# Performance work log

Measured on AMD Instinct MI355X. Metric: run time of the kernel, lower is better.

## Reference

```python
import jax, jax.numpy as jnp
import numpy as np

N_NODES = 50000
N_EDGES = 800000
IN_CH = 128
OUT_CH = 32
HEADS = 8
NEG_SLOPE = 0.2


def setup_inputs() -> dict:
    key = jax.random.key(0)
    k1, k2, k3, k4, k5, k6 = jax.random.split(key, 6)
    x = jax.random.normal(k1, (N_NODES, IN_CH), dtype=jnp.float32)
    edge_index = jax.random.randint(k2, (2, N_EDGES), 0, N_NODES, dtype=jnp.int64)
    # Glorot-ish scaled params
    W = jax.random.normal(k3, (IN_CH, HEADS * OUT_CH), dtype=jnp.float32) * (1.0 / np.sqrt(IN_CH))
    att_src = jax.random.normal(k4, (HEADS, OUT_CH), dtype=jnp.float32) * (1.0 / np.sqrt(OUT_CH))
    att_dst = jax.random.normal(k5, (HEADS, OUT_CH), dtype=jnp.float32) * (1.0 / np.sqrt(OUT_CH))
    bias = jax.random.normal(k6, (HEADS * OUT_CH,), dtype=jnp.float32) * 0.01
    return {"x": x, "edge_index": edge_index, "W": W, "att_src": att_src, "att_dst": att_dst, "bias": bias}


def reference(x, edge_index, W, att_src, att_dst, bias):
    N = x.shape[0]
    # PyG GATConv default: add self loops
    loops = jnp.arange(N, dtype=edge_index.dtype)
    src = jnp.concatenate([edge_index[0], loops])  # message source j
    dst = jnp.concatenate([edge_index[1], loops])  # message destination i

    # Linear projection: [N, H, C]
    h = (x @ W).reshape(N, HEADS, OUT_CH)

    # Per-node attention logits per head: [N, H]
    a_src = jnp.einsum('nhc,hc->nh', h, att_src)
    a_dst = jnp.einsum('nhc,hc->nh', h, att_dst)

    # Per-edge scores: [E, H]
    e = jax.nn.leaky_relu(a_src[src] + a_dst[dst], NEG_SLOPE)

    # Segment softmax over edges sharing a destination (self loops guarantee non-empty segments)
    e_max = jax.ops.segment_max(e, dst, num_segments=N)
    e_exp = jnp.exp(e - e_max[dst])
    e_sum = jax.ops.segment_sum(e_exp, dst, num_segments=N)
    alpha = e_exp / (e_sum[dst] + 1e-16)  # [E, H]

    # Weighted message aggregation: [N, H, C] -> concat heads [N, H*C]
    msg = h[src] * alpha[:, :, None]
    out = jax.ops.segment_sum(msg, dst, num_segments=N).reshape(N, HEADS * OUT_CH)
    out = out + bias
    # unlinear = ReLU (act='relu', norm=None)
    return jax.nn.relu(out)
```

## Files before the change

### kernel.cpp

```cpp
#include <hip/hip_runtime.h>

#define IN_CH 128
#define OUT_CH 32
#define HEADS 8
#define HC 256
#define NEG_SLOPE 0.2f

typedef __attribute__((ext_vector_type(8))) short short8;
typedef __attribute__((ext_vector_type(4))) float f32x4;

__device__ __forceinline__ float bflo(unsigned u) { return __uint_as_float(u << 16); }
__device__ __forceinline__ float bfhi(unsigned u) { return __uint_as_float(u & 0xffff0000u); }
__device__ __forceinline__ float bf2f(unsigned short u) { return __uint_as_float(((unsigned)u) << 16); }
__device__ __forceinline__ unsigned short f2bf(float f) {
    unsigned u = __float_as_uint(f);
    u = (u + 0x7fffu + ((u >> 16) & 1u)) >> 16;
    return (unsigned short)u;
}

__global__ __launch_bounds__(256)
void gat_prep(const float* __restrict__ W, unsigned short* __restrict__ Wt,
              int* __restrict__ counts, int n)
{
    const int idx = blockIdx.x * 256 + threadIdx.x;
    const int k = idx >> 8;
    const int col = idx & 255;
    Wt[col * IN_CH + k] = f2bf(W[idx]);
    for (int i = idx; i < n; i += 32768) counts[i] = 0;
}

__global__ __launch_bounds__(256)
void gat_proj_mfma(const float* __restrict__ x, const unsigned short* __restrict__ Wt,
                   const float* __restrict__ attS, const float* __restrict__ attD,
                   unsigned short* __restrict__ h, float* __restrict__ aS,
                   float* __restrict__ aD, int N)
{
    __shared__ unsigned short lbuf[32 * 264];

    const int tid = threadIdx.x;
    const int lane = tid & 63;
    const int w = tid >> 6;
    const int row0 = blockIdx.x * 32;

#pragma unroll
    for (int u = 0; u < 2; ++u) {
        const int unit = tid + u * 256;
        const int srow = unit >> 4;
        const int sseg = unit & 15;
        const int grow = row0 + srow;
        float4 v0 = make_float4(0.f, 0.f, 0.f, 0.f), v1 = v0;
        if (grow < N) {
            const float* xp = x + (size_t)grow * IN_CH + sseg * 8;
            v0 = *(const float4*)xp;
            v1 = *(const float4*)(xp + 4);
        }
        short8 pk;
        pk[0] = (short)f2bf(v0.x); pk[1] = (short)f2bf(v0.y);
        pk[2] = (short)f2bf(v0.z); pk[3] = (short)f2bf(v0.w);
        pk[4] = (short)f2bf(v1.x); pk[5] = (short)f2bf(v1.y);
        pk[6] = (short)f2bf(v1.z); pk[7] = (short)f2bf(v1.w);
        *(short8*)&lbuf[srow * 136 + sseg * 8] = pk;
    }
    __syncthreads();

    const unsigned short* wp = Wt + (size_t)(w * 64 + (lane & 15)) * IN_CH
                                  + ((lane >> 4) << 3);

    f32x4 acc[2][4];
#pragma unroll
    for (int m = 0; m < 2; ++m)
#pragma unroll
        for (int i = 0; i < 4; ++i) acc[m][i] = (f32x4){0.f, 0.f, 0.f, 0.f};

#pragma unroll
    for (int ks = 0; ks < 4; ++ks) {
        short8 bfr[4];
#pragma unroll
        for (int i = 0; i < 4; ++i)
            bfr[i] = *(const short8*)(wp + i * 16 * IN_CH + ks * 32);
#pragma unroll
        for (int m = 0; m < 2; ++m) {
            const short8 a = *(const short8*)&lbuf[((lane & 15) + m * 16) * 136
                                                   + ks * 32 + ((lane >> 4) << 3)];
#pragma unroll
            for (int i = 0; i < 4; ++i)
                acc[m][i] = __builtin_amdgcn_mfma_f32_16x16x32_bf16(a, bfr[i], acc[m][i], 0, 0, 0);
        }
    }

    const int rbase = (lane >> 4) << 2;
    float ps[2][2][4], pd[2][2][4];
#pragma unroll
    for (int m = 0; m < 2; ++m)
#pragma unroll
        for (int hp = 0; hp < 2; ++hp)
#pragma unroll
            for (int r = 0; r < 4; ++r) { ps[m][hp][r] = 0.f; pd[m][hp][r] = 0.f; }

#pragma unroll
    for (int i = 0; i < 4; ++i) {
        const int hp = i >> 1;
        const float asv = attS[(w * 2 + hp) * 32 + (i & 1) * 16 + (lane & 15)];
        const float adv = attD[(w * 2 + hp) * 32 + (i & 1) * 16 + (lane & 15)];
#pragma unroll
        for (int m = 0; m < 2; ++m)
#pragma unroll
            for (int r = 0; r < 4; ++r) {
                ps[m][hp][r] = fmaf(acc[m][i][r], asv, ps[m][hp][r]);
                pd[m][hp][r] = fmaf(acc[m][i][r], adv, pd[m][hp][r]);
            }
    }
#pragma unroll
    for (int off = 1; off < 16; off <<= 1) {
#pragma unroll
        for (int m = 0; m < 2; ++m)
#pragma unroll
            for (int hp = 0; hp < 2; ++hp)
#pragma unroll
                for (int r = 0; r < 4; ++r) {
                    ps[m][hp][r] += __shfl_xor(ps[m][hp][r], off, 64);
                    pd[m][hp][r] += __shfl_xor(pd[m][hp][r], off, 64);
                }
    }
    if ((lane & 15) == 0) {
#pragma unroll
        for (int m = 0; m < 2; ++m)
#pragma unroll
            for (int hp = 0; hp < 2; ++hp)
#pragma unroll
                for (int r = 0; r < 4; ++r) {
                    const int grow = row0 + m * 16 + rbase + r;
                    if (grow < N) {
                        aS[grow * HEADS + w * 2 + hp] = ps[m][hp][r];
                        aD[grow * HEADS + w * 2 + hp] = pd[m][hp][r];
                    }
                }
    }

    __syncthreads();
#pragma unroll
    for (int i = 0; i < 4; ++i) {
        const int col = w * 64 + i * 16 + (lane & 15);
#pragma unroll
        for (int m = 0; m < 2; ++m)
#pragma unroll
            for (int r = 0; r < 4; ++r)
                lbuf[(m * 16 + rbase + r) * 264 + col] = f2bf(acc[m][i][r]);
    }
    __syncthreads();

#pragma unroll
    for (int u = 0; u < 4; ++u) {
        const int unit = u * 256 + tid;
        const int srow = unit >> 5;
        const int sseg = unit & 31;
        const int grow = row0 + srow;
        if (grow < N)
            *(short8*)(h + (size_t)grow * HC + sseg * 8) =
                *(const short8*)&lbuf[srow * 264 + sseg * 8];
    }
}

__global__ __launch_bounds__(256)
void gat_hist(const int* __restrict__ dst, int* __restrict__ counts,
              int* __restrict__ rank, int E)
{
    int i = (blockIdx.x * 256 + threadIdx.x) * 8;
    if (i + 7 < E) {
        const int4 d0 = *(const int4*)&dst[i];
        const int4 d1 = *(const int4*)&dst[i + 4];
        int4 r0, r1;
        r0.x = atomicAdd(&counts[d0.x], 1);
        r0.y = atomicAdd(&counts[d0.y], 1);
        r0.z = atomicAdd(&counts[d0.z], 1);
        r0.w = atomicAdd(&counts[d0.w], 1);
        r1.x = atomicAdd(&counts[d1.x], 1);
        r1.y = atomicAdd(&counts[d1.y], 1);
        r1.z = atomicAdd(&counts[d1.z], 1);
        r1.w = atomicAdd(&counts[d1.w], 1);
        *(int4*)&rank[i] = r0;
        *(int4*)&rank[i + 4] = r1;
    } else {
        for (; i < E; ++i) rank[i] = atomicAdd(&counts[dst[i]], 1);
    }
}

__global__ __launch_bounds__(256)
void gat_scan1(const int* __restrict__ counts, int* __restrict__ bsum, int n)
{
    __shared__ int ws[4];
    const int t = threadIdx.x;
    const int lane = t & 63;
    const int wid = t >> 6;
    const int idx = blockIdx.x * 1024 + t * 4;
    int4 v = {0, 0, 0, 0};
    if (idx + 3 < n) v = *(const int4*)&counts[idx];
    else {
        if (idx < n)     v.x = counts[idx];
        if (idx + 1 < n) v.y = counts[idx + 1];
        if (idx + 2 < n) v.z = counts[idx + 2];
    }
    int s4 = v.x + v.y + v.z + v.w;
#pragma unroll
    for (int off = 1; off < 64; off <<= 1) s4 += __shfl_xor(s4, off, 64);
    if (lane == 0) ws[wid] = s4;
    __syncthreads();
    if (t == 0) bsum[blockIdx.x] = ws[0] + ws[1] + ws[2] + ws[3];
}

__global__ __launch_bounds__(256)
void gat_scan3(const int* __restrict__ counts, const int* __restrict__ bsum,
               int* __restrict__ offsets, int n, int nb, int E)
{
    __shared__ int wsums[4];
    __shared__ int bbase_s;
    const int t = threadIdx.x;
    const int lane = t & 63;
    const int wid = t >> 6;

    if (t < 64) {
        const int v = (t < nb) ? bsum[t] : 0;
        int inc = v;
#pragma unroll
        for (int off = 1; off < 64; off <<= 1) {
            const int y = __shfl_up(inc, off, 64);
            if (t >= off) inc += y;
        }
        const int myv   = __shfl(v, blockIdx.x, 64);
        const int myinc = __shfl(inc, blockIdx.x, 64);
        if (t == 0) bbase_s = myinc - myv;
    }

    const int idx = blockIdx.x * 1024 + t * 4;
    int4 v = {0, 0, 0, 0};
    if (idx + 3 < n) v = *(const int4*)&counts[idx];
    else {
        if (idx < n)     v.x = counts[idx];
        if (idx + 1 < n) v.y = counts[idx + 1];
        if (idx + 2 < n) v.z = counts[idx + 2];
    }
    const int s4 = v.x + v.y + v.z + v.w;
    int inc = s4;
#pragma unroll
    for (int off = 1; off < 64; off <<= 1) {
        const int y = __shfl_up(inc, off, 64);
        if (lane >= off) inc += y;
    }
    if (lane == 63) wsums[wid] = inc;
    __syncthreads();
    int wbase = 0;
    for (int i = 0; i < wid; ++i) wbase += wsums[i];
    const int base = bbase_s + wbase + (inc - s4);
    int4 o;
    o.x = base;
    o.y = base + v.x;
    o.z = o.y + v.y;
    o.w = o.z + v.z;
    if (idx + 3 < n) {
        *(int4*)&offsets[idx] = o;
    } else {
        if (idx < n)     offsets[idx] = o.x;
        if (idx + 1 < n) offsets[idx + 1] = o.y;
        if (idx + 2 < n) offsets[idx + 2] = o.z;
    }
    if (blockIdx.x == 0 && t == 0) offsets[n] = E;
}

__global__ __launch_bounds__(256)
void gat_scatter(const int* __restrict__ src, const int* __restrict__ dst,
                 const int* __restrict__ rank, const int* __restrict__ offsets,
                 int* __restrict__ ssrc, unsigned short* __restrict__ ealpha,
                 const float* __restrict__ aS, const float* __restrict__ aD, int E)
{
    const int e = blockIdx.x * 256 + threadIdx.x;
    if (e >= E) return;
    const int s = src[e];
    const int d = dst[e];
    const int pos = offsets[d] + rank[e];
    ssrc[pos] = s;
    const float4 s0 = *(const float4*)(aS + (size_t)s * HEADS);
    const float4 s1 = *(const float4*)(aS + (size_t)s * HEADS + 4);
    const float4 d0 = *(const float4*)(aD + (size_t)d * HEADS);
    const float4 d1 = *(const float4*)(aD + (size_t)d * HEADS + 4);
    float lg[8] = { s0.x + d0.x, s0.y + d0.y, s0.z + d0.z, s0.w + d0.w,
                    s1.x + d1.x, s1.y + d1.y, s1.z + d1.z, s1.w + d1.w };
    short8 al;
#pragma unroll
    for (int k = 0; k < 8; ++k) {
        const float v = lg[k] > 0.f ? lg[k] : NEG_SLOPE * lg[k];
        al[k] = (short)f2bf(__expf(v));
    }
    *(short8*)(ealpha + (size_t)pos * HEADS) = al;
}

__global__ __launch_bounds__(256)
void gat_agg(const unsigned short* __restrict__ h,
             const float* __restrict__ aS, const float* __restrict__ aD,
             const int* __restrict__ offsets, const int* __restrict__ ssrc,
             const unsigned short* __restrict__ ealpha,
             const float* __restrict__ bias, float* __restrict__ out, int N)
{
    const int t = threadIdx.x;
    const int lane = t & 63;
    const int node = blockIdx.x * 4 + (t >> 6);
    if (node >= N) return;

    const int half = lane >> 5;
    const int hl = lane & 31;
    const int head = hl >> 2;
    const int ch = head * 32 + (hl & 3) * 8;

    float sum;
    float acc[8];
    {
        float lg0 = aS[node * HEADS + head] + aD[node * HEADS + head];
        lg0 = (lg0 > 0.f) ? lg0 : NEG_SLOPE * lg0;
        const float w0 = half ? 0.f : __expf(lg0);
        sum = w0;
        const uint4 hv = *(const uint4*)(h + (size_t)node * HC + ch);
        acc[0] = w0 * bflo(hv.x); acc[1] = w0 * bfhi(hv.x);
        acc[2] = w0 * bflo(hv.y); acc[3] = w0 * bfhi(hv.y);
        acc[4] = w0 * bflo(hv.z); acc[5] = w0 * bfhi(hv.z);
        acc[6] = w0 * bflo(hv.w); acc[7] = w0 * bfhi(hv.w);
    }

    const int beg = offsets[node];
    const int end = offsets[node + 1];
    const int last = end - 1;

    int sE[4];
    float aE[4];
#pragma unroll
    for (int j = 0; j < 4; ++j) { sE[j] = node; aE[j] = 0.f; }

    if (beg < end) {
#pragma unroll
        for (int j = 0; j < 4; ++j) {
            const int e = beg + half * 4 + j;
            const int c = min(e, last);
            int s = ssrc[c];
            float a = bf2f(ealpha[(size_t)c * HEADS + head]);
            if (e > last) { s = node; a = 0.f; }
            sE[j] = s; aE[j] = a;
        }
    }

    for (int base = beg; base < end; base += 8) {
        int tS[4]; float tA[4];
#pragma unroll
        for (int j = 0; j < 4; ++j) {
            const int e = base + 8 + half * 4 + j;
            const int c = min(e, last);
            int s = ssrc[c];
            float a = bf2f(ealpha[(size_t)c * HEADS + head]);
            if (e > last) { s = node; a = 0.f; }
            tS[j] = s; tA[j] = a;
        }
        uint4 v[4];
#pragma unroll
        for (int j = 0; j < 4; ++j)
            v[j] = *(const uint4*)(h + (size_t)sE[j] * HC + ch);
#pragma unroll
        for (int j = 0; j < 4; ++j) {
            const float a = aE[j];
            sum += a;
            acc[0] = fmaf(a, bflo(v[j].x), acc[0]);
            acc[1] = fmaf(a, bfhi(v[j].x), acc[1]);
            acc[2] = fmaf(a, bflo(v[j].y), acc[2]);
            acc[3] = fmaf(a, bfhi(v[j].y), acc[3]);
            acc[4] = fmaf(a, bflo(v[j].z), acc[4]);
            acc[5] = fmaf(a, bfhi(v[j].z), acc[5]);
            acc[6] = fmaf(a, bflo(v[j].w), acc[6]);
            acc[7] = fmaf(a, bfhi(v[j].w), acc[7]);
        }
#pragma unroll
        for (int j = 0; j < 4; ++j) { sE[j] = tS[j]; aE[j] = tA[j]; }
    }

#pragma unroll
    for (int j = 0; j < 8; ++j) acc[j] += __shfl_xor(acc[j], 32, 64);
    sum += __shfl_xor(sum, 32, 64);

    const float inv = 1.f / (sum + 1e-16f);
    const int cbase = ch + half * 4;
    const int j0 = half * 4;
    const float4 bv = *(const float4*)(bias + cbase);
    float4 o;
    o.x = fmaxf(fmaf(acc[j0 + 0], inv, bv.x), 0.f);
    o.y = fmaxf(fmaf(acc[j0 + 1], inv, bv.y), 0.f);
    o.z = fmaxf(fmaf(acc[j0 + 2], inv, bv.z), 0.f);
    o.w = fmaxf(fmaf(acc[j0 + 3], inv, bv.w), 0.f);
    *(float4*)(out + (size_t)node * HC + cbase) = o;
}

extern "C" void kernel_launch(void* const* d_in, const int* in_sizes, int n_in,
                              void* d_out, int out_size, void* d_ws, size_t ws_size,
                              hipStream_t stream)
{
    const float* x    = (const float*)d_in[0];
    const int*   ei   = (const int*)d_in[1];
    const float* W    = (const float*)d_in[2];
    const float* attS = (const float*)d_in[3];
    const float* attD = (const float*)d_in[4];
    const float* bias = (const float*)d_in[5];
    float* out = (float*)d_out;

    const int N = in_sizes[0] / IN_CH;
    const int E = in_sizes[1] / 2;
    const int* esrc = ei;
    const int* edst = ei + E;

    unsigned short* h = (unsigned short*)d_ws;
    float* aS = (float*)(h + (size_t)N * HC);
    float* aD = aS + (size_t)N * HEADS;
    int* counts  = (int*)(aD + (size_t)N * HEADS);
    int* offsets = counts + N;
    int* rank    = offsets + (N + 4);
    int* ssrc    = rank + E;
    int* bsum    = ssrc + E;
    unsigned short* Wt = (unsigned short*)(bsum + 64);
    unsigned short* ealpha = Wt + IN_CH * HC;

    const int nb = (N + 1023) / 1024;

    gat_prep<<<(IN_CH * HC) / 256, 256, 0, stream>>>(W, Wt, counts, N);
    gat_proj_mfma<<<(N + 31) / 32, 256, 0, stream>>>(x, Wt, attS, attD, h, aS, aD, N);
    gat_hist<<<(E / 8 + 255) / 256, 256, 0, stream>>>(edst, counts, rank, E);
    gat_scan1<<<nb, 256, 0, stream>>>(counts, bsum, N);
    gat_scan3<<<nb, 256, 0, stream>>>(counts, bsum, offsets, N, nb, E);
    gat_scatter<<<(E + 255) / 256, 256, 0, stream>>>(esrc, edst, rank, offsets, ssrc, ealpha, aS, aD, E);
    gat_agg<<<(N + 3) / 4, 256, 0, stream>>>(h, aS, aD, offsets, ssrc, ealpha, bias, out, N);
}
```

Baseline: 177.2 us.

## Fuse weight prep with histogram and compute attention logits via MFMA

```diff
diff --git a/kernel.cpp b/kernel.cpp
--- a/kernel.cpp
+++ b/kernel.cpp
@@ -19,153 +19,29 @@
 }
 
 __global__ __launch_bounds__(256)
-void gat_prep(const float* __restrict__ W, unsigned short* __restrict__ Wt,
-              int* __restrict__ counts, int n)
-{
-    const int idx = blockIdx.x * 256 + threadIdx.x;
-    const int k = idx >> 8;
-    const int col = idx & 255;
-    Wt[col * IN_CH + k] = f2bf(W[idx]);
-    for (int i = idx; i < n; i += 32768) counts[i] = 0;
-}
-
-__global__ __launch_bounds__(256)
-void gat_proj_mfma(const float* __restrict__ x, const unsigned short* __restrict__ Wt,
+void gat_prep_hist(const float* __restrict__ W, unsigned short* __restrict__ Wt,
                    const float* __restrict__ attS, const float* __restrict__ attD,
-                   unsigned short* __restrict__ h, float* __restrict__ aS,
-                   float* __restrict__ aD, int N)
-{
-    __shared__ unsigned short lbuf[32 * 264];
-
+                   unsigned short* __restrict__ Blt,
+                   const int* __restrict__ dst, int* __restrict__ counts,
+                   int* __restrict__ rank, int E)
+{
     const int tid = threadIdx.x;
-    const int lane = tid & 63;
-    const int w = tid >> 6;
-    const int row0 = blockIdx.x * 32;
-
-#pragma unroll
-    for (int u = 0; u < 2; ++u) {
-        const int unit = tid + u * 256;
-        const int srow = unit >> 4;
-        const int sseg = unit & 15;
-        const int grow = row0 + srow;
-        float4 v0 = make_float4(0.f, 0.f, 0.f, 0.f), v1 = v0;
-        if (grow < N) {
-            const float* xp = x + (size_t)grow * IN_CH + sseg * 8;
-            v0 = *(const float4*)xp;
-            v1 = *(const float4*)(xp + 4);
-        }
-        short8 pk;
-        pk[0] = (short)f2bf(v0.x); pk[1] = (short)f2bf(v0.y);
-        pk[2] = (short)f2bf(v0.z); pk[3] = (short)f2bf(v0.w);
-        pk[4] = (short)f2bf(v1.x); pk[5] = (short)f2bf(v1.y);
-        pk[6] = (short)f2bf(v1.z); pk[7] = (short)f2bf(v1.w);
-        *(short8*)&lbuf[srow * 136 + sseg * 8] = pk;
-    }
-    __syncthreads();
-
-    const unsigned short* wp = Wt + (size_t)(w * 64 + (lane & 15)) * IN_CH
-                                  + ((lane >> 4) << 3);
-
-    f32x4 acc[2][4];
-#pragma unroll
-    for (int m = 0; m < 2; ++m)
-#pragma unroll
-        for (int i = 0; i < 4; ++i) acc[m][i] = (f32x4){0.f, 0.f, 0.f, 0.f};
-
-#pragma unroll
-    for (int ks = 0; ks < 4; ++ks) {
-        short8 bfr[4];
-#pragma unroll
-        for (int i = 0; i < 4; ++i)
-            bfr[i] = *(const short8*)(wp + i * 16 * IN_CH + ks * 32);
-#pragma unroll
-        for (int m = 0; m < 2; ++m) {
-            const short8 a = *(const short8*)&lbuf[((lane & 15) + m * 16) * 136
-                                                   + ks * 32 + ((lane >> 4) << 3)];
-#pragma unroll
-            for (int i = 0; i < 4; ++i)
-                acc[m][i] = __builtin_amdgcn_mfma_f32_16x16x32_bf16(a, bfr[i], acc[m][i], 0, 0, 0);
-        }
-    }
-
-    const int rbase = (lane >> 4) << 2;
-    float ps[2][2][4], pd[2][2][4];
-#pragma unroll
-    for (int m = 0; m < 2; ++m)
-#pragma unroll
-        for (int hp = 0; hp < 2; ++hp)
-#pragma unroll
-            for (int r = 0; r < 4; ++r) { ps[m][hp][r] = 0.f; pd[m][hp][r] = 0.f; }
-
-#pragma unroll
-    for (int i = 0; i < 4; ++i) {
-        const int hp = i >> 1;
-        const float asv = attS[(w * 2 + hp) * 32 + (i & 1) * 16 + (lane & 15)];
-        const float adv = attD[(w * 2 + hp) * 32 + (i & 1) * 16 + (lane & 15)];
-#pragma unroll
-        for (int m = 0; m < 2; ++m)
-#pragma unroll
-            for (int r = 0; r < 4; ++r) {
-                ps[m][hp][r] = fmaf(acc[m][i][r], asv, ps[m][hp][r]);
-                pd[m][hp][r] = fmaf(acc[m][i][r], adv, pd[m][hp][r]);
-            }
-    }
-#pragma unroll
-    for (int off = 1; off < 16; off <<= 1) {
-#pragma unroll
-        for (int m = 0; m < 2; ++m)
-#pragma unroll
-            for (int hp = 0; hp < 2; ++hp)
-#pragma unroll
-                for (int r = 0; r < 4; ++r) {
-                    ps[m][hp][r] += __shfl_xor(ps[m][hp][r], off, 64);
-                    pd[m][hp][r] += __shfl_xor(pd[m][hp][r], off, 64);
-                }
-    }
-    if ((lane & 15) == 0) {
-#pragma unroll
-        for (int m = 0; m < 2; ++m)
-#pragma unroll
-            for (int hp = 0; hp < 2; ++hp)
-#pragma unroll
-                for (int r = 0; r < 4; ++r) {
-                    const int grow = row0 + m * 16 + rbase + r;
-                    if (grow < N) {
-                        aS[grow * HEADS + w * 2 + hp] = ps[m][hp][r];
-                        aD[grow * HEADS + w * 2 + hp] = pd[m][hp][r];
-                    }
-                }
-    }
-
-    __syncthreads();
-#pragma unroll
-    for (int i = 0; i < 4; ++i) {
-        const int col = w * 64 + i * 16 + (lane & 15);
-#pragma unroll
-        for (int m = 0; m < 2; ++m)
-#pragma unroll
-            for (int r = 0; r < 4; ++r)
-                lbuf[(m * 16 + rbase + r) * 264 + col] = f2bf(acc[m][i][r]);
-    }
-    __syncthreads();
-
-#pragma unroll
-    for (int u = 0; u < 4; ++u) {
-        const int unit = u * 256 + tid;
-        const int srow = unit >> 5;
-        const int sseg = unit & 31;
-        const int grow = row0 + srow;
-        if (grow < N)
-            *(short8*)(h + (size_t)grow * HC + sseg * 8) =
-                *(const short8*)&lbuf[srow * 264 + sseg * 8];
-    }
-}
-
-__global__ __launch_bounds__(256)
-void gat_hist(const int* __restrict__ dst, int* __restrict__ counts,
-              int* __restrict__ rank, int E)
-{
-    int i = (blockIdx.x * 256 + threadIdx.x) * 8;
+    if (blockIdx.x < 128) {
+        const int idx = blockIdx.x * 256 + tid;
+        const int k = idx >> 8;
+        const int col = idx & 255;
+        Wt[col * IN_CH + k] = f2bf(W[idx]);
+        if (idx < 16 * HC) {
+            const int j = idx >> 8;
+            const int kk = idx & 255;
+            float v = 0.f;
+            if (j < 8)  v = ((kk >> 5) == j)       ? attS[kk] : 0.f;
+            else        v = ((kk >> 5) == (j - 8)) ? attD[kk] : 0.f;
+            Blt[j * HC + kk] = f2bf(v);
+        }
+        return;
+    }
+    int i = ((blockIdx.x - 128) * 256 + tid) * 8;
     if (i + 7 < E) {
         const int4 d0 = *(const int4*)&dst[i];
         const int4 d1 = *(const int4*)&dst[i + 4];
@@ -186,6 +62,121 @@
 }
 
 __global__ __launch_bounds__(256)
+void gat_proj_mfma(const float* __restrict__ x, const unsigned short* __restrict__ Wt,
+                   const unsigned short* __restrict__ Blt,
+                   unsigned short* __restrict__ h, float* __restrict__ aSD, int N)
+{
+    __shared__ unsigned short lbuf[32 * 264];
+    __shared__ float red[4][2][16][16];
+
+    const int tid = threadIdx.x;
+    const int lane = tid & 63;
+    const int w = tid >> 6;
+    const int row0 = blockIdx.x * 32;
+
+#pragma unroll
+    for (int u = 0; u < 2; ++u) {
+        const int unit = tid + u * 256;
+        const int srow = unit >> 4;
+        const int sseg = unit & 15;
+        const int grow = row0 + srow;
+        float4 v0 = make_float4(0.f, 0.f, 0.f, 0.f), v1 = v0;
+        if (grow < N) {
+            const float* xp = x + (size_t)grow * IN_CH + sseg * 8;
+            v0 = *(const float4*)xp;
+            v1 = *(const float4*)(xp + 4);
+        }
+        short8 pk;
+        pk[0] = (short)f2bf(v0.x); pk[1] = (short)f2bf(v0.y);
+        pk[2] = (short)f2bf(v0.z); pk[3] = (short)f2bf(v0.w);
+        pk[4] = (short)f2bf(v1.x); pk[5] = (short)f2bf(v1.y);
+        pk[6] = (short)f2bf(v1.z); pk[7] = (short)f2bf(v1.w);
+        *(short8*)&lbuf[srow * 136 + sseg * 8] = pk;
+    }
+    __syncthreads();
+
+    const unsigned short* wp = Wt + (size_t)(w * 64 + (lane & 15)) * IN_CH
+                                  + ((lane >> 4) << 3);
+
+    f32x4 acc[2][4];
+#pragma unroll
+    for (int m = 0; m < 2; ++m)
+#pragma unroll
+        for (int i = 0; i < 4; ++i) acc[m][i] = (f32x4){0.f, 0.f, 0.f, 0.f};
+
+#pragma unroll
+    for (int ks = 0; ks < 4; ++ks) {
+        short8 bfr[4];
+#pragma unroll
+        for (int i = 0; i < 4; ++i)
+            bfr[i] = *(const short8*)(wp + i * 16 * IN_CH + ks * 32);
+#pragma unroll
+        for (int m = 0; m < 2; ++m) {
+            const short8 a = *(const short8*)&lbuf[((lane & 15) + m * 16) * 136
+                                                   + ks * 32 + ((lane >> 4) << 3)];
+#pragma unroll
+            for (int i = 0; i < 4; ++i)
+                acc[m][i] = __builtin_amdgcn_mfma_f32_16x16x32_bf16(a, bfr[i], acc[m][i], 0, 0, 0);
+        }
+    }
+
+    __syncthreads();
+    const int rbase = (lane >> 4) << 2;
+#pragma unroll
+    for (int i = 0; i < 4; ++i) {
+        const int col = w * 64 + i * 16 + (lane & 15);
+#pragma unroll
+        for (int m = 0; m < 2; ++m)
+#pragma unroll
+            for (int r = 0; r < 4; ++r)
+                lbuf[(m * 16 + rbase + r) * 264 + col] = f2bf(acc[m][i][r]);
+    }
+    __syncthreads();
+
+#pragma unroll
+    for (int u = 0; u < 4; ++u) {
+        const int unit = u * 256 + tid;
+        const int srow = unit >> 5;
+        const int sseg = unit & 31;
+        const int grow = row0 + srow;
+        if (grow < N)
+            *(short8*)(h + (size_t)grow * HC + sseg * 8) =
+                *(const short8*)&lbuf[srow * 264 + sseg * 8];
+    }
+
+    f32x4 cl[2] = {{0.f,0.f,0.f,0.f},{0.f,0.f,0.f,0.f}};
+#pragma unroll
+    for (int kl = 0; kl < 2; ++kl) {
+        const int ks = w * 2 + kl;
+        const short8 b = *(const short8*)(Blt + (lane & 15) * HC + ks * 32 + ((lane >> 4) << 3));
+#pragma unroll
+        for (int m = 0; m < 2; ++m) {
+            const short8 a = *(const short8*)&lbuf[((lane & 15) + m * 16) * 264
+                                                   + ks * 32 + ((lane >> 4) << 3)];
+            cl[m] = __builtin_amdgcn_mfma_f32_16x16x32_bf16(a, b, cl[m], 0, 0, 0);
+        }
+    }
+#pragma unroll
+    for (int m = 0; m < 2; ++m)
+#pragma unroll
+        for (int r = 0; r < 4; ++r)
+            red[w][m][rbase + r][lane & 15] = cl[m][r];
+    __syncthreads();
+
+#pragma unroll
+    for (int u = 0; u < 2; ++u) {
+        const int o = u * 256 + tid;
+        const int m = o >> 8;
+        const int row = (o >> 4) & 15;
+        const int j = o & 15;
+        const float s = red[0][m][row][j] + red[1][m][row][j]
+                      + red[2][m][row][j] + red[3][m][row][j];
+        const int grow = row0 + m * 16 + row;
+        if (grow < N) aSD[grow * 16 + j] = s;
+    }
+}
+
+__global__ __launch_bounds__(256)
 void gat_scan1(const int* __restrict__ counts, int* __restrict__ bsum, int n)
 {
     __shared__ int ws[4];
@@ -270,7 +261,7 @@
 void gat_scatter(const int* __restrict__ src, const int* __restrict__ dst,
                  const int* __restrict__ rank, const int* __restrict__ offsets,
                  int* __restrict__ ssrc, unsigned short* __restrict__ ealpha,
-                 const float* __restrict__ aS, const float* __restrict__ aD, int E)
+                 const float* __restrict__ aSD, int E)
 {
     const int e = blockIdx.x * 256 + threadIdx.x;
     if (e >= E) return;
@@ -278,10 +269,10 @@
     const int d = dst[e];
     const int pos = offsets[d] + rank[e];
     ssrc[pos] = s;
-    const float4 s0 = *(const float4*)(aS + (size_t)s * HEADS);
-    const float4 s1 = *(const float4*)(aS + (size_t)s * HEADS + 4);
-    const float4 d0 = *(const float4*)(aD + (size_t)d * HEADS);
-    const float4 d1 = *(const float4*)(aD + (size_t)d * HEADS + 4);
+    const float4 s0 = *(const float4*)(aSD + (size_t)s * 16);
+    const float4 s1 = *(const float4*)(aSD + (size_t)s * 16 + 4);
+    const float4 d0 = *(const float4*)(aSD + (size_t)d * 16 + 8);
+    const float4 d1 = *(const float4*)(aSD + (size_t)d * 16 + 12);
     float lg[8] = { s0.x + d0.x, s0.y + d0.y, s0.z + d0.z, s0.w + d0.w,
                     s1.x + d1.x, s1.y + d1.y, s1.z + d1.z, s1.w + d1.w };
     short8 al;
@@ -294,8 +285,7 @@
 }
 
 __global__ __launch_bounds__(256)
-void gat_agg(const unsigned short* __restrict__ h,
-             const float* __restrict__ aS, const float* __restrict__ aD,
+void gat_agg(const unsigned short* __restrict__ h, const float* __restrict__ aSD,
              const int* __restrict__ offsets, const int* __restrict__ ssrc,
              const unsigned short* __restrict__ ealpha,
              const float* __restrict__ bias, float* __restrict__ out, int N)
@@ -313,7 +303,7 @@
     float sum;
     float acc[8];
     {
-        float lg0 = aS[node * HEADS + head] + aD[node * HEADS + head];
+        float lg0 = aSD[(size_t)node * 16 + head] + aSD[(size_t)node * 16 + 8 + head];
         lg0 = (lg0 > 0.f) ? lg0 : NEG_SLOPE * lg0;
         const float w0 = half ? 0.f : __expf(lg0);
         sum = w0;
@@ -411,23 +401,25 @@
     const int* edst = ei + E;
 
     unsigned short* h = (unsigned short*)d_ws;
-    float* aS = (float*)(h + (size_t)N * HC);
-    float* aD = aS + (size_t)N * HEADS;
-    int* counts  = (int*)(aD + (size_t)N * HEADS);
+    float* aSD = (float*)(h + (size_t)N * HC);
+    int* counts  = (int*)(aSD + (size_t)N * 16);
     int* offsets = counts + N;
     int* rank    = offsets + (N + 4);
     int* ssrc    = rank + E;
     int* bsum    = ssrc + E;
     unsigned short* Wt = (unsigned short*)(bsum + 64);
-    unsigned short* ealpha = Wt + IN_CH * HC;
+    unsigned short* Blt = Wt + IN_CH * HC;
+    unsigned short* ealpha = Blt + 16 * HC;
 
     const int nb = (N + 1023) / 1024;
-
-    gat_prep<<<(IN_CH * HC) / 256, 256, 0, stream>>>(W, Wt, counts, N);
-    gat_proj_mfma<<<(N + 31) / 32, 256, 0, stream>>>(x, Wt, attS, attD, h, aS, aD, N);
-    gat_hist<<<(E / 8 + 255) / 256, 256, 0, stream>>>(edst, counts, rank, E);
+    const int histBlocks = (E / 8 + 255) / 256;
+
+    hipMemsetAsync(counts, 0, (size_t)N * sizeof(int), stream);
+    gat_prep_hist<<<128 + histBlocks, 256, 0, stream>>>(
+        W, Wt, attS, attD, Blt, edst, counts, rank, E);
+    gat_proj_mfma<<<(N + 31) / 32, 256, 0, stream>>>(x, Wt, Blt, h, aSD, N);
     gat_scan1<<<nb, 256, 0, stream>>>(counts, bsum, N);
     gat_scan3<<<nb, 256, 0, stream>>>(counts, bsum, offsets, N, nb, E);
-    gat_scatter<<<(E + 255) / 256, 256, 0, stream>>>(esrc, edst, rank, offsets, ssrc, ealpha, aS, aD, E);
-    gat_agg<<<(N + 3) / 4, 256, 0, stream>>>(h, aS, aD, offsets, ssrc, ealpha, bias, out, N);
-}
+    gat_scatter<<<(E + 255) / 256, 256, 0, stream>>>(esrc, edst, rank, offsets, ssrc, ealpha, aSD, E);
+    gat_agg<<<(N + 3) / 4, 256, 0, stream>>>(h, aSD, offsets, ssrc, ealpha, bias, out, N);
+}
```

After: 173.2 us, median of 2. 2.3% less time.
